# Optimization experiments

Measured on AMD Instinct MI355X. Metric: run time of the kernel, lower is better.

The kernel has to match this reference:

```python
import jax, jax.numpy as jnp
import numpy as np

BLOCKSIZE = 4096
OUT_FEATURES = 16384
IN_FEATURES = 4096
BATCH, SEQ = 4, 2048


def setup_inputs() -> dict:
    key = jax.random.key(0)
    k_x, k_w, k_a, k_b = jax.random.split(key, 4)
    x = jax.random.normal(k_x, (BATCH, SEQ, IN_FEATURES), dtype=jnp.float32)
    # quantized int8 weight stored as indices into the 256-entry codebook
    weight_q = jax.random.randint(k_w, (OUT_FEATURES, IN_FEATURES), 0, 256, dtype=jnp.int32)
    n_blocks = (OUT_FEATURES * IN_FEATURES) // BLOCKSIZE  # 16384
    absmax = jax.random.uniform(k_a, (n_blocks,), dtype=jnp.float32) + 0.5
    # bitsandbytes dynamic-map code: a sorted table of values in [-1, 1]
    code = jnp.linspace(-1.0, 1.0, 256, dtype=jnp.float32)
    bias = jax.random.normal(k_b, (OUT_FEATURES,), dtype=jnp.float32) * 0.02
    return {"x": x, "weight_q": weight_q, "absmax": absmax, "code": code, "bias": bias}


def dequantize_blockwise(weight_q, absmax, code):
    # codebook lookup then per-block absmax scaling
    flat = code[weight_q.reshape(-1)]                      # [out*in]
    flat = flat.reshape(-1, BLOCKSIZE) * absmax[:, None]   # [n_blocks, blocksize]
    return flat.reshape(weight_q.shape)                    # [out, in]


def reference(x, weight_q, absmax, code, bias):
    w = dequantize_blockwise(weight_q, absmax, code)       # [out, in] fp32
    # F.linear(x, w, bias) = x @ w.T + bias
    return jnp.einsum("bsi,oi->bso", x, w) + bias
```

## Files before the change

kernel.cpp:

```cpp
#include <hip/hip_runtime.h>
#include <hip/hip_bf16.h>
#include <stdint.h>

#define M_TOTAL 8192
#define N_TOTAL 16384
#define K_TOTAL 4096

#define BM 256
#define BN 256
#define BK 64
#define NKT (K_TOTAL / BK)

using f32x4  = __attribute__((ext_vector_type(4))) float;
using bf16x8 = __attribute__((ext_vector_type(8))) short;

#define UNROLL _Pragma("unroll")

__device__ __forceinline__ unsigned short f2bf(float f) {
    union { float f; unsigned u; } v; v.f = f;
    unsigned r = v.u + 0x7fffu + ((v.u >> 16) & 1u);
    return (unsigned short)(r >> 16);
}

__device__ __forceinline__ void gload_lds16(const void* g, void* l) {
    __builtin_amdgcn_global_load_lds(
        (const __attribute__((address_space(1))) unsigned int*)g,
        (__attribute__((address_space(3))) unsigned int*)l,
        16, 0, 0);
}

__global__ void dequant_w_kernel(const int* __restrict__ q,
                                 const float* __restrict__ am,
                                 const float* __restrict__ code,
                                 unsigned short* __restrict__ wb) {
    __shared__ float lc[256];
    if (threadIdx.x < 256) lc[threadIdx.x] = code[threadIdx.x];
    __syncthreads();
    const int total = (N_TOTAL / 4) * K_TOTAL;
    const int stride = gridDim.x * blockDim.x;
    for (int i = blockIdx.x * blockDim.x + threadIdx.x; i < total; i += stride) {
        int4 v = reinterpret_cast<const int4*>(q)[i];
        float a = am[i >> 10];
        ushort4 o;
        o.x = f2bf(lc[v.x & 255] * a);
        o.y = f2bf(lc[v.y & 255] * a);
        o.z = f2bf(lc[v.z & 255] * a);
        o.w = f2bf(lc[v.w & 255] * a);
        reinterpret_cast<ushort4*>(wb)[i] = o;
    }
}

__global__ void cvt_x_kernel(const float* __restrict__ x,
                             unsigned short* __restrict__ xb) {
    const int total = (M_TOTAL * K_TOTAL) / 4;
    const int stride = gridDim.x * blockDim.x;
    for (int i = blockIdx.x * blockDim.x + threadIdx.x; i < total; i += stride) {
        float4 v = reinterpret_cast<const float4*>(x)[i];
        ushort4 o;
        o.x = f2bf(v.x); o.y = f2bf(v.y); o.z = f2bf(v.z); o.w = f2bf(v.w);
        reinterpret_cast<ushort4*>(xb)[i] = o;
    }
}

#define LOAD_A(DST, BUFI, MH)                                                     \
    UNROLL for (int mf = 0; mf < 4; ++mf)                                         \
        UNROLL for (int ks = 0; ks < 2; ++ks)                                     \
            DST[mf][ks] = *reinterpret_cast<const bf16x8*>(                       \
                &sA[BUFI][((MH)*128 + arow_base + mf*16)*BK +                     \
                          (((ks*4 + rslot_hi) ^ rslot_xor)*8)]);

#define LOAD_B(DST, BUFI, NH)                                                     \
    UNROLL for (int nf = 0; nf < 2; ++nf)                                         \
        UNROLL for (int ks = 0; ks < 2; ++ks)                                     \
            DST[nf][ks] = *reinterpret_cast<const bf16x8*>(                       \
                &sB[BUFI][((NH)*128 + brow_base + nf*16)*BK +                     \
                          (((ks*4 + rslot_hi) ^ rslot_xor)*8)]);

#define MFMA_Q(MH, NH, AR, BR)                                                    \
    UNROLL for (int mf = 0; mf < 4; ++mf)                                         \
        UNROLL for (int nf = 0; nf < 2; ++nf) {                                   \
            acc[MH][mf][NH][nf] = __builtin_amdgcn_mfma_f32_16x16x32_bf16(        \
                AR[mf][0], BR[nf][0], acc[MH][mf][NH][nf], 0, 0, 0);              \
            acc[MH][mf][NH][nf] = __builtin_amdgcn_mfma_f32_16x16x32_bf16(        \
                AR[mf][1], BR[nf][1], acc[MH][mf][NH][nf], 0, 0, 0);              \
        }

#define PH_BAR()                                                                  \
    asm volatile("s_waitcnt lgkmcnt(0)" ::: "memory");                            \
    __builtin_amdgcn_s_barrier();                                                 \
    asm volatile("" ::: "memory");

#define TILE2(BUF, AH1T, TS)                                                      \
    LOAD_A(a_r, BUF, 0); LOAD_B(b0_r, BUF, 0); LOAD_B(b1_r, BUF, 1);              \
    if ((AH1T) >= 0) { stA(1,0,AH1T,(BUF)^1); stA(1,1,AH1T,(BUF)^1); }            \
    __builtin_amdgcn_s_setprio(1);                                                \
    MFMA_Q(0, 0, a_r, b0_r);                                                      \
    MFMA_Q(0, 1, a_r, b1_r);                                                      \
    __builtin_amdgcn_s_setprio(0);                                                \
    PH_BAR();                                                                     \
    LOAD_A(a_r, BUF, 1);                                                          \
    if ((TS) >= 0) { stA(0,0,TS,BUF); stA(0,1,TS,BUF);                            \
                     stB(0,0,TS,BUF); stB(0,1,TS,BUF);                            \
                     stB(1,0,TS,BUF); stB(1,1,TS,BUF); }                          \
    __builtin_amdgcn_s_setprio(1);                                                \
    MFMA_Q(1, 1, a_r, b1_r);                                                      \
    MFMA_Q(1, 0, a_r, b0_r);                                                      \
    __builtin_amdgcn_s_setprio(0);

#define GATE(VMN)                                                                 \
    asm volatile("s_waitcnt lgkmcnt(0) vmcnt(" #VMN ")" ::: "memory");            \
    __builtin_amdgcn_s_barrier();                                                 \
    asm volatile("" ::: "memory");

__global__ __launch_bounds__(512, 2) void gemm_p2_kernel(
        const unsigned short* __restrict__ A,
        const unsigned short* __restrict__ B,
        const float* __restrict__ bias,
        float* __restrict__ C) {
    __shared__ __align__(16) unsigned short sA[2][BM * BK];
    __shared__ __align__(16) unsigned short sB[2][BN * BK];

    const int nwg = gridDim.x;
    const int bid = blockIdx.x;
    const int wg  = (bid & 7) * (nwg >> 3) + (bid >> 3);
    const int nbn = N_TOTAL / BN;
    const int brow = (wg / nbn) * BM;
    const int bcol = (wg % nbn) * BN;

    const int tid  = threadIdx.x;
    const int wid  = tid >> 6;
    const int lane = tid & 63;
    const int wm   = wid >> 2;
    const int wn   = wid & 3;

    const int srow = wid * 8 + (lane >> 3);
    const int scol = ((lane & 7) ^ (lane >> 3)) * 8;
    const unsigned short* Asrc = A + (long long)(brow + srow) * K_TOTAL + scol;
    const unsigned short* Bsrc = B + (long long)(bcol + srow) * K_TOTAL + scol;

    auto stA = [&](int h, int j, int kt, int b) {
        gload_lds16(Asrc + (long long)(h*128 + j*64) * K_TOTAL + kt*BK,
                    &sA[b][(h*128 + j*64)*BK + wid*512]);
    };
    auto stB = [&](int h, int j, int kt, int b) {
        gload_lds16(Bsrc + (long long)(h*128 + j*64) * K_TOTAL + kt*BK,
                    &sB[b][(h*128 + j*64)*BK + wid*512]);
    };

    const int arow_base = wm * 64 + (lane & 15);
    const int brow_base = wn * 32 + (lane & 15);
    const int rslot_hi  = lane >> 4;
    const int rslot_xor = lane & 7;

    f32x4 acc[2][4][2][2];
    UNROLL for (int mh = 0; mh < 2; ++mh)
        UNROLL for (int mf = 0; mf < 4; ++mf)
            UNROLL for (int nh = 0; nh < 2; ++nh)
                UNROLL for (int nf = 0; nf < 2; ++nf)
                    acc[mh][mf][nh][nf] = (f32x4){0.f, 0.f, 0.f, 0.f};

    bf16x8 a_r[4][2];
    bf16x8 b0_r[2][2], b1_r[2][2];

    stA(0,0,0,0); stA(0,1,0,0); stA(1,0,0,0); stA(1,1,0,0);
    stB(0,0,0,0); stB(0,1,0,0); stB(1,0,0,0); stB(1,1,0,0);
    stA(0,0,1,1); stA(0,1,1,1);
    stB(0,0,1,1); stB(0,1,1,1); stB(1,0,1,1); stB(1,1,1,1);
    asm volatile("s_waitcnt vmcnt(6)" ::: "memory");
    __builtin_amdgcn_s_barrier();
    asm volatile("" ::: "memory");

    for (int it = 0; it < NKT/2 - 1; ++it) {
        const int t0 = 2*it;
        TILE2(0, t0 + 1, t0 + 2)
        GATE(6)
        TILE2(1, t0 + 2, t0 + 3)
        GATE(6)
    }
    TILE2(0, 63, -1)
    GATE(0)
    TILE2(1, -1, -1)

    const int crow0 = (lane >> 4) * 4;
    const int ccol  = lane & 15;
    UNROLL for (int mh = 0; mh < 2; ++mh)
        UNROLL for (int mf = 0; mf < 4; ++mf) {
            const long long row0 = (long long)brow + mh*128 + wm*64 + mf*16 + crow0;
            UNROLL for (int nh = 0; nh < 2; ++nh)
                UNROLL for (int nf = 0; nf < 2; ++nf) {
                    const int col = bcol + nh*128 + wn*32 + nf*16 + ccol;
                    const float bv = bias[col];
                    UNROLL for (int r = 0; r < 4; ++r)
                        C[(row0 + r) * N_TOTAL + col] = acc[mh][mf][nh][nf][r] + bv;
                }
        }
}

extern "C" void kernel_launch(void* const* d_in, const int* in_sizes, int n_in,
                              void* d_out, int out_size, void* d_ws, size_t ws_size,
                              hipStream_t stream) {
    const float* x      = (const float*)d_in[0];
    const int*   wq     = (const int*)  d_in[1];
    const float* absmax = (const float*)d_in[2];
    const float* code   = (const float*)d_in[3];
    const float* bias   = (const float*)d_in[4];
    float* out = (float*)d_out;

    unsigned short* wb = (unsigned short*)d_ws;
    unsigned short* xb = wb + (size_t)N_TOTAL * K_TOTAL;

    dequant_w_kernel<<<2048, 256, 0, stream>>>(wq, absmax, code, wb);
    cvt_x_kernel   <<<2048, 256, 0, stream>>>(x, xb);

    dim3 grid((M_TOTAL / BM) * (N_TOTAL / BN));
    gemm_p2_kernel<<<grid, 512, 0, stream>>>(xb, wb, bias, out);
}
```

Measured before the change: 1.113 ms.

## Prefetch next-tile LDS fragments into registers during current tile MFMAs

Restructures the GEMM main loop so the A/B register fragments for the next K tile are read from LDS while the current tile's MFMAs run. It uses split a0/a1 register sets and loads B fragments between MFMA quarters, and drops the lgkmcnt(0) waits from the barriers. The aim is to hide LDS read latency behind matrix math and shorten barrier stalls. In exchange it raises register pressure under launch_bounds(512,2). The relaxed waitcnt ordering could also cause races or spills if mis-sequenced.

```diff
diff --git a/kernel.cpp b/kernel.cpp
--- a/kernel.cpp
+++ b/kernel.cpp
@@ -85,34 +85,38 @@
                 AR[mf][1], BR[nf][1], acc[MH][mf][NH][nf], 0, 0, 0);              \
         }
 
-#define PH_BAR()                                                                  \
-    asm volatile("s_waitcnt lgkmcnt(0)" ::: "memory");                            \
+#define P1_BAR()                                                                  \
+    asm volatile("s_waitcnt vmcnt(2)" ::: "memory");                              \
     __builtin_amdgcn_s_barrier();                                                 \
     asm volatile("" ::: "memory");
 
-#define TILE2(BUF, AH1T, TS)                                                      \
-    LOAD_A(a_r, BUF, 0); LOAD_B(b0_r, BUF, 0); LOAD_B(b1_r, BUF, 1);              \
+#define GATE(VMN)                                                                 \
+    asm volatile("s_waitcnt vmcnt(" #VMN ")" ::: "memory");                       \
+    __builtin_amdgcn_s_barrier();                                                 \
+    asm volatile("" ::: "memory");
+
+#define TILE_PF(BUF, AH1T, TS, LDN)                                               \
+    LOAD_A(a1_r, BUF, 1);                                                         \
     if ((AH1T) >= 0) { stA(1,0,AH1T,(BUF)^1); stA(1,1,AH1T,(BUF)^1); }            \
     __builtin_amdgcn_s_setprio(1);                                                \
-    MFMA_Q(0, 0, a_r, b0_r);                                                      \
-    MFMA_Q(0, 1, a_r, b1_r);                                                      \
+    MFMA_Q(0, 0, a0_r, b0_r);                                                     \
+    MFMA_Q(0, 1, a0_r, b1_r);                                                     \
     __builtin_amdgcn_s_setprio(0);                                                \
-    PH_BAR();                                                                     \
-    LOAD_A(a_r, BUF, 1);                                                          \
+    P1_BAR();                                                                     \
+    if (LDN) { LOAD_A(a0_r, (BUF)^1, 0); }                                        \
     if ((TS) >= 0) { stA(0,0,TS,BUF); stA(0,1,TS,BUF);                            \
                      stB(0,0,TS,BUF); stB(0,1,TS,BUF);                            \
                      stB(1,0,TS,BUF); stB(1,1,TS,BUF); }                          \
     __builtin_amdgcn_s_setprio(1);                                                \
-    MFMA_Q(1, 1, a_r, b1_r);                                                      \
-    MFMA_Q(1, 0, a_r, b0_r);                                                      \
-    __builtin_amdgcn_s_setprio(0);
-
-#define GATE(VMN)                                                                 \
-    asm volatile("s_waitcnt lgkmcnt(0) vmcnt(" #VMN ")" ::: "memory");            \
-    __builtin_amdgcn_s_barrier();                                                 \
-    asm volatile("" ::: "memory");
-
-__global__ __launch_bounds__(512, 2) void gemm_p2_kernel(
+    MFMA_Q(1, 1, a1_r, b1_r);                                                     \
+    __builtin_amdgcn_s_setprio(0);                                                \
+    if (LDN) { LOAD_B(b1_r, (BUF)^1, 1); }                                        \
+    __builtin_amdgcn_s_setprio(1);                                                \
+    MFMA_Q(1, 0, a1_r, b0_r);                                                     \
+    __builtin_amdgcn_s_setprio(0);                                                \
+    if (LDN) { LOAD_B(b0_r, (BUF)^1, 0); }
+
+__global__ __launch_bounds__(512, 2) void gemm_pf_kernel(
         const unsigned short* __restrict__ A,
         const unsigned short* __restrict__ B,
         const float* __restrict__ bias,
@@ -159,7 +163,7 @@
                 UNROLL for (int nf = 0; nf < 2; ++nf)
                     acc[mh][mf][nh][nf] = (f32x4){0.f, 0.f, 0.f, 0.f};
 
-    bf16x8 a_r[4][2];
+    bf16x8 a0_r[4][2], a1_r[4][2];
     bf16x8 b0_r[2][2], b1_r[2][2];
 
     stA(0,0,0,0); stA(0,1,0,0); stA(1,0,0,0); stA(1,1,0,0);
@@ -169,17 +173,20 @@
     asm volatile("s_waitcnt vmcnt(6)" ::: "memory");
     __builtin_amdgcn_s_barrier();
     asm volatile("" ::: "memory");
+    LOAD_A(a0_r, 0, 0);
+    LOAD_B(b0_r, 0, 0);
+    LOAD_B(b1_r, 0, 1);
 
     for (int it = 0; it < NKT/2 - 1; ++it) {
         const int t0 = 2*it;
-        TILE2(0, t0 + 1, t0 + 2)
+        TILE_PF(0, t0 + 1, t0 + 2, 1)
         GATE(6)
-        TILE2(1, t0 + 2, t0 + 3)
+        TILE_PF(1, t0 + 2, t0 + 3, 1)
         GATE(6)
     }
-    TILE2(0, 63, -1)
+    TILE_PF(0, 63, -1, 1)
     GATE(0)
-    TILE2(1, -1, -1)
+    TILE_PF(1, -1, -1, 0)
 
     const int crow0 = (lane >> 4) * 4;
     const int ccol  = lane & 15;
@@ -213,5 +220,5 @@
     cvt_x_kernel   <<<2048, 256, 0, stream>>>(x, xb);
 
     dim3 grid((M_TOTAL / BM) * (N_TOTAL / BN));
-    gemm_p2_kernel<<<grid, 512, 0, stream>>>(xb, wb, bias, out);
-}
+    gemm_pf_kernel<<<grid, 512, 0, stream>>>(xb, wb, bias, out);
+}
```

Result: slower. 1.213 ms (+8.9%).
